# Optimization experiments

Hardware: AMD Instinct MI355X
Metric: run time of the kernel (lower is better)

The kernel has to match this reference:

```python
import jax, jax.numpy as jnp
import numpy as np

EMB = 128   # embedding_dim
ND = 128    # node_dim
B = 64      # graphs in batch
NN = 500    # n_nodes per graph
N = B * NN  # total nodes = 32000
E = 256000  # edges per edge set
M = 20      # history length in input_


def _lin_params(key, out_dim, in_dim, bias=True):
    k1, k2 = jax.random.split(key)
    s = 1.0 / np.sqrt(in_dim)
    w = jax.random.uniform(k1, (out_dim, in_dim), jnp.float32, -s, s)
    if bias:
        b = jax.random.uniform(k2, (out_dim,), jnp.float32, -s, s)
        return w, b
    return w


def setup_inputs() -> dict:
    key = jax.random.key(0)
    ks = jax.random.split(key, 40)
    inp = {}
    inp["state_"] = jax.random.normal(ks[0], (B, ND), jnp.float32)
    inp["input_"] = jax.random.normal(ks[1], (B, M, EMB), jnp.float32)
    inp["x"] = jax.random.normal(ks[2], (N, EMB), jnp.float32)
    inp["e_n"] = jax.random.randint(ks[3], (2, E), 0, N)
    inp["e_r0"] = jax.random.randint(ks[4], (2, E), 0, N)
    inp["e_r1"] = jax.random.randint(ks[5], (2, E), 0, N)
    inp["n_nodes"] = NN
    # GRU-like params
    inp["win"] = _lin_params(ks[6], ND, EMB, bias=False)
    inp["wz"], inp["bz"] = _lin_params(ks[7], ND, 2 * ND)
    inp["wr"], inp["br"] = _lin_params(ks[8], ND, 2 * ND)
    inp["wh"], inp["bh"] = _lin_params(ks[9], ND, 2 * ND)
    # GAT params: lin (out,in)+bias, attn (out, 2*out)+bias
    inp["g0_lw"], inp["g0_lb"] = _lin_params(ks[10], ND, EMB)
    inp["g0_aw"], inp["g0_ab"] = _lin_params(ks[11], ND, 2 * ND)
    inp["g1_lw"], inp["g1_lb"] = _lin_params(ks[12], ND, ND)
    inp["g1_aw"], inp["g1_ab"] = _lin_params(ks[13], ND, 2 * ND)
    inp["g2_lw"], inp["g2_lb"] = _lin_params(ks[14], ND, ND)
    inp["g2_aw"], inp["g2_ab"] = _lin_params(ks[15], ND, 2 * ND)
    inp["gn_lw"], inp["gn_lb"] = _lin_params(ks[16], ND, ND)
    inp["gn_aw"], inp["gn_ab"] = _lin_params(ks[17], ND, 2 * ND)
    # heads
    inp["pw"], inp["pb"] = _lin_params(ks[18], 1, ND)
    inp["mw"], inp["mb"] = _lin_params(ks[19], 1, ND)
    inp["sw"], inp["sb"] = _lin_params(ks[20], 1, ND)
    return inp


def gat_conv(x, ei, lw, lb, aw, ab, slope=0.2):
    """PyG GATConv variant: lin -> per-edge attn(cat(x_i,x_j)) -> leaky_relu ->
    per-dst segment softmax (per channel) -> scatter-add of x_j*alpha."""
    n = x.shape[0]
    sl = jnp.arange(n)
    src = jnp.concatenate([ei[0], sl])   # j (source)
    dst = jnp.concatenate([ei[1], sl])   # i (target; softmax + aggregation index)
    h = x @ lw.T + lb                    # [N, ND]
    hi = h[dst]                          # x_i  [E', ND]
    hj = h[src]                          # x_j  [E', ND]
    a = jnp.concatenate([hi, hj], axis=-1) @ aw.T + ab
    a = jax.nn.leaky_relu(a, slope)
    amax = jax.ops.segment_max(a, dst, num_segments=n)
    e = jnp.exp(a - amax[dst])
    denom = jax.ops.segment_sum(e, dst, num_segments=n)
    alpha = e / (denom[dst] + 1e-16)
    return jax.ops.segment_sum(hj * alpha, dst, num_segments=n)


def reference(state_, input_, x, e_n, e_r0, e_r1, n_nodes,
              win, wz, bz, wr, br, wh, bh,
              g0_lw, g0_lb, g0_aw, g0_ab,
              g1_lw, g1_lb, g1_aw, g1_ab,
              g2_lw, g2_lb, g2_aw, g2_ab,
              gn_lw, gn_lb, gn_aw, gn_ab,
              pw, pb, mw, mb, sw, sb):
    # GRU-like gated state update
    st = state_.reshape(-1, ND)
    inp = input_.reshape(st.shape[0], -1, EMB)
    i = jnp.mean(inp @ win.T, axis=1)              # [B, ND]
    si = jnp.concatenate([st, i], axis=-1)
    z = jax.nn.sigmoid(si @ wz.T + bz)
    r = jax.nn.sigmoid(si @ wr.T + br)
    hc = jnp.tanh(jnp.concatenate([r * st, i], axis=-1) @ wh.T + bh)
    h = (1 - z) * st + z * hc                      # [B, ND]

    # Stacked GAT layers
    g0 = gat_conv(x, e_n, g0_lw, g0_lb, g0_aw, g0_ab)
    g1 = gat_conv(g0, e_r1, g1_lw, g1_lb, g1_aw, g1_ab)
    g2 = gat_conv(g1, e_r1, g1_lw, g1_lb, g1_aw, g1_ab)
    g3 = gat_conv(g2, e_n, gn_lw, gn_lb, gn_aw, gn_ab) + g0
    g4 = gat_conv(g3, e_r0, g2_lw, g2_lb, g2_aw, g2_ab)
    g5 = gat_conv(g4, e_r0, g2_lw, g2_lb, g2_aw, g2_ab)
    gx = gat_conv(g5, e_n, gn_lw, gn_lb, gn_aw, gn_ab) + g3

    xg = gx.reshape(-1, n_nodes, ND)               # [B, NN, ND]
    xt = xg[:, 1:]                                 # skip depot node
    scores = (xt @ pw.T + pb)[..., 0]              # [B, NN-1]
    probs = jax.nn.softmax(scores, axis=-1)        # Categorical params
    a = jax.nn.elu((xt @ mw.T + mb)[..., 0]) + 2   # Beta alpha
    b = jax.nn.elu(jnp.abs((xt @ sw.T + sb)[..., 0])) + 2  # Beta beta
    return (h, probs, a, b)
```

## Files before the change

kernel.cpp:

```cpp
#include <hip/hip_runtime.h>
#include <hip/hip_bf16.h>

#define ND 128
#define EMB 128
#define BATCH 64
#define MM 20
#define NN 500
#define RPAD 8

typedef short bf16x8 __attribute__((ext_vector_type(8)));
typedef float f32x4 __attribute__((ext_vector_type(4)));

__device__ __forceinline__ float bf2f(unsigned short u) {
    union { unsigned int i; float f; } x; x.i = ((unsigned int)u) << 16; return x.f;
}
__device__ __forceinline__ unsigned short f2bf(float f) {
    union { float f; unsigned int i; } x; x.f = f;
    unsigned int r = x.i + 0x7fffu + ((x.i >> 16) & 1u);
    return (unsigned short)(r >> 16);
}
__device__ __forceinline__ float2 bfpair(unsigned int p) {
    union { unsigned int i; float f; } a, b;
    a.i = p << 16; b.i = p & 0xffff0000u;
    return make_float2(a.f, b.f);
}

struct EdgePtrs { const int* e[3]; };

__global__ void edge_hist3(EdgePtrs ep, int* __restrict__ cnt, int E, int N) {
    int li = blockIdx.y;
    const int* dst = ep.e[li] + E;
    int e = blockIdx.x * blockDim.x + threadIdx.x;
    if (e < E) atomicAdd(&cnt[(size_t)li * N + dst[e]], 1);
}

__global__ void exscan3(const int* __restrict__ cnt, int* __restrict__ rowptr, int n) {
    __shared__ int wsum[16];
    __shared__ int woff[16];
    int li = blockIdx.x;
    const int4* c4 = (const int4*)(cnt + (size_t)li * n);
    int* rp = rowptr + (size_t)li * (n + RPAD);
    int t = threadIdx.x;
    int lane = t & 63, wid = t >> 6;
    int n4 = n >> 2;

    int4 v[8];
    int s = 0;
#pragma unroll
    for (int i = 0; i < 8; ++i) {
        int idx = t * 8 + i;
        if (idx < n4) v[i] = c4[idx];
        else { v[i].x = v[i].y = v[i].z = v[i].w = 0; }
    }
#pragma unroll
    for (int i = 0; i < 8; ++i) s += v[i].x + v[i].y + v[i].z + v[i].w;

    int ps = s;
#pragma unroll
    for (int d = 1; d < 64; d <<= 1) {
        int u = __shfl_up(ps, d, 64);
        if (lane >= d) ps += u;
    }
    if (lane == 63) wsum[wid] = ps;
    __syncthreads();
    if (t == 0) {
        int r = 0;
        for (int i = 0; i < 16; ++i) { woff[i] = r; r += wsum[i]; }
    }
    __syncthreads();
    int run = woff[wid] + ps - s;
    int4* rp4 = (int4*)rp;
#pragma unroll
    for (int i = 0; i < 8; ++i) {
        int idx = t * 8 + i;
        if (idx < n4) {
            int4 o;
            o.x = run; run += v[i].x;
            o.y = run; run += v[i].y;
            o.z = run; run += v[i].z;
            o.w = run; run += v[i].w;
            rp4[idx] = o;
        }
    }
    if (t == (n - 1) / 32) rp[n] = run;
}

__global__ void edge_scatter3(EdgePtrs ep, const int* __restrict__ rowptr, int* __restrict__ cnt,
                              int* __restrict__ col, int E, int N) {
    int li = blockIdx.y;
    const int* src = ep.e[li];
    const int* dst = src + E;
    const int* rp = rowptr + (size_t)li * (N + RPAD);
    int e = blockIdx.x * blockDim.x + threadIdx.x;
    if (e < E) {
        int d = dst[e];
        int p = atomicSub(&cnt[(size_t)li * N + d], 1) - 1;
        col[(size_t)li * E + rp[d] + p] = src[e];
    }
}

struct WcPtrs {
    const float* lw[4]; const float* lb[4]; const float* aw[4]; const float* ab[4];
    unsigned short* Whi[4]; unsigned short* Wlo[4]; float* Bf[4];
};

__global__ void make_wc4(WcPtrs p) {
    int set = blockIdx.y;
    const float* lw = p.lw[set]; const float* lb = p.lb[set];
    const float* aw = p.aw[set]; const float* ab = p.ab[set];
    int n = blockIdx.x;
    int e = threadIdx.x;
    float w;
    if (n < 128) {
        w = lw[n * 128 + e];
    } else if (n < 256) {
        int ni = n - 128; float s = 0.f;
        for (int k = 0; k < 128; ++k) s += aw[ni * 256 + k] * lw[k * 128 + e];
        w = s;
    } else {
        int nj = n - 256; float s = 0.f;
        for (int k = 0; k < 128; ++k) s += aw[nj * 256 + 128 + k] * lw[k * 128 + e];
        w = s;
    }
    unsigned short hi = f2bf(w);
    p.Whi[set][n * 128 + e] = hi;
    p.Wlo[set][n * 128 + e] = f2bf(w - bf2f(hi));
    if (e == 0) {
        float b;
        if (n < 128) b = lb[n];
        else if (n < 256) {
            int ni = n - 128; float s = ab[ni];
            for (int k = 0; k < 128; ++k) s += aw[ni * 256 + k] * lb[k];
            b = s;
        } else {
            int nj = n - 256; float s = 0.f;
            for (int k = 0; k < 128; ++k) s += aw[nj * 256 + 128 + k] * lb[k];
            b = s;
        }
        p.Bf[set][n] = b;
    }
}

__launch_bounds__(768, 3)
__global__ void lin_fused(const float* __restrict__ X,
                          const unsigned short* __restrict__ Whi,
                          const unsigned short* __restrict__ Wlo,
                          const float* __restrict__ bias,
                          void* __restrict__ hu, int M) {
    __shared__ __align__(16) unsigned short sxh[2][16][136];
    __shared__ __align__(16) unsigned short sxl[2][16][136];
    const int tid = threadIdx.x;
    const int wave = tid >> 6;
    const int lane = tid & 63;
    const int r16 = lane & 15;
    const int quad = lane >> 4;
    const int srow = tid >> 4;
    const int scol = (tid & 15) * 8;

    unsigned short* hu16 = (unsigned short*)hu;
    float* huf = (float*)hu;

    bf16x8 wh[2][4], wl[2][4];
#pragma unroll
    for (int nt = 0; nt < 2; ++nt)
#pragma unroll
        for (int ks = 0; ks < 4; ++ks) {
            size_t wrow = (size_t)(wave * 32 + nt * 16 + r16) * 128 + ks * 32 + quad * 8;
            wh[nt][ks] = *(const bf16x8*)(Whi + wrow);
            wl[nt][ks] = *(const bf16x8*)(Wlo + wrow);
        }
    float bv[2];
#pragma unroll
    for (int nt = 0; nt < 2; ++nt) bv[nt] = bias[wave * 32 + nt * 16 + r16];

    const int mt_count = M >> 4;
    const int G = gridDim.x;
    const int mt0 = blockIdx.x;

    {
        float v[8];
        if (tid < 256) {
            const float* xp = X + (size_t)(mt0 * 16 + srow) * 128 + scol;
            float4 v0 = *(const float4*)xp;
            float4 v1 = *(const float4*)(xp + 4);
            v[0] = v0.x; v[1] = v0.y; v[2] = v0.z; v[3] = v0.w;
            v[4] = v1.x; v[5] = v1.y; v[6] = v1.z; v[7] = v1.w;
            unsigned int hh[4], ll[4];
#pragma unroll
            for (int j = 0; j < 4; ++j) {
                unsigned short h0 = f2bf(v[2 * j]);
                unsigned short h1 = f2bf(v[2 * j + 1]);
                unsigned short l0 = f2bf(v[2 * j] - bf2f(h0));
                unsigned short l1 = f2bf(v[2 * j + 1] - bf2f(h1));
                hh[j] = (unsigned int)h0 | ((unsigned int)h1 << 16);
                ll[j] = (unsigned int)l0 | ((unsigned int)l1 << 16);
            }
            *(uint4*)&sxh[0][srow][scol] = make_uint4(hh[0], hh[1], hh[2], hh[3]);
            *(uint4*)&sxl[0][srow][scol] = make_uint4(ll[0], ll[1], ll[2], ll[3]);
        }
    }
    __syncthreads();

    int cur = 0;
    for (int mt = mt0; mt < mt_count; mt += G) {
        const int nxt = mt + G;
        const bool has = nxt < mt_count;

        float v[8];
        if (has && tid < 256) {
            const float* xp = X + (size_t)(nxt * 16 + srow) * 128 + scol;
            float4 v0 = *(const float4*)xp;
            float4 v1 = *(const float4*)(xp + 4);
            v[0] = v0.x; v[1] = v0.y; v[2] = v0.z; v[3] = v0.w;
            v[4] = v1.x; v[5] = v1.y; v[6] = v1.z; v[7] = v1.w;
        }

        bf16x8 ah[4], al[4];
#pragma unroll
        for (int ks = 0; ks < 4; ++ks) {
            ah[ks] = *(const bf16x8*)&sxh[cur][r16][ks * 32 + quad * 8];
            al[ks] = *(const bf16x8*)&sxl[cur][r16][ks * 32 + quad * 8];
        }

#pragma unroll
        for (int nt = 0; nt < 2; ++nt) {
            f32x4 acc = {bv[nt], bv[nt], bv[nt], bv[nt]};
#pragma unroll
            for (int ks = 0; ks < 4; ++ks) {
                acc = __builtin_amdgcn_mfma_f32_16x16x32_bf16(ah[ks], wh[nt][ks], acc, 0, 0, 0);
                acc = __builtin_amdgcn_mfma_f32_16x16x32_bf16(al[ks], wh[nt][ks], acc, 0, 0, 0);
                acc = __builtin_amdgcn_mfma_f32_16x16x32_bf16(ah[ks], wl[nt][ks], acc, 0, 0, 0);
            }
            int cc = wave * 32 + nt * 16 + r16;
#pragma unroll
            for (int r = 0; r < 4; ++r) {
                size_t row = (size_t)(mt * 16 + quad * 4 + r);
                if (cc < 128) {
                    hu16[row * 512 + ((cc & ~1) << 1) + (cc & 1)] = f2bf(acc[r]);
                } else if (cc < 256) {
                    int c = cc - 128;
                    huf[row * 256 + 128 + c] = acc[r];
                } else {
                    int c = cc - 256;
                    hu16[row * 512 + ((c & ~1) << 1) + 2 + (c & 1)] = f2bf(acc[r]);
                }
            }
        }

        if (has && tid < 256) {
            unsigned int hh[4], ll[4];
#pragma unroll
            for (int j = 0; j < 4; ++j) {
                unsigned short h0 = f2bf(v[2 * j]);
                unsigned short h1 = f2bf(v[2 * j + 1]);
                unsigned short l0 = f2bf(v[2 * j] - bf2f(h0));
                unsigned short l1 = f2bf(v[2 * j + 1] - bf2f(h1));
                hh[j] = (unsigned int)h0 | ((unsigned int)h1 << 16);
                ll[j] = (unsigned int)l0 | ((unsigned int)l1 << 16);
            }
            *(uint4*)&sxh[cur ^ 1][srow][scol] = make_uint4(hh[0], hh[1], hh[2], hh[3]);
            *(uint4*)&sxl[cur ^ 1][srow][scol] = make_uint4(ll[0], ll[1], ll[2], ll[3]);
        }
        __syncthreads();
        cur ^= 1;
    }
}

__global__ void gat_agg(const void* __restrict__ hu,
                        const int* __restrict__ rowptr, const int* __restrict__ col,
                        const float* __restrict__ resid,
                        float* __restrict__ out, int N) {
    int wid = (int)((blockIdx.x * blockDim.x + threadIdx.x) >> 6);
    if (wid >= N) return;
    int lane = threadIdx.x & 63;
    const uint2* P = (const uint2*)hu;
    const float2* U = (const float2*)hu;

    float2 uiv = U[(size_t)wid * 128 + 64 + lane];
    uint2 sp = P[(size_t)wid * 128 + lane];
    float2 hs = bfpair(sp.x);
    float2 ujs = bfpair(sp.y);

    float a0 = uiv.x + ujs.x; a0 = a0 > 0.f ? a0 : 0.2f * a0;
    float a1 = uiv.y + ujs.y; a1 = a1 > 0.f ? a1 : 0.2f * a1;
    float m0 = a0, m1 = a1, l0 = 1.f, l1 = 1.f;
    float acc0 = hs.x, acc1 = hs.y;

#define AGG_STEP(pk)                                                      \
    {                                                                     \
        float2 hj = bfpair(pk.x);                                         \
        float2 uj = bfpair(pk.y);                                         \
        float b0 = uiv.x + uj.x; b0 = b0 > 0.f ? b0 : 0.2f * b0;          \
        float b1 = uiv.y + uj.y; b1 = b1 > 0.f ? b1 : 0.2f * b1;          \
        float n0 = fmaxf(m0, b0), n1 = fmaxf(m1, b1);                     \
        float s0 = __expf(m0 - n0), s1 = __expf(m1 - n1);                 \
        float p0 = __expf(b0 - n0), p1 = __expf(b1 - n1);                 \
        l0 = l0 * s0 + p0;            l1 = l1 * s1 + p1;                  \
        acc0 = acc0 * s0 + hj.x * p0; acc1 = acc1 * s1 + hj.y * p1;       \
        m0 = n0; m1 = n1;                                                 \
    }

    int e = rowptr[wid], end = rowptr[wid + 1];
    for (; e + 8 <= end; e += 8) {
        int s0i = col[e],     s1i = col[e + 1], s2i = col[e + 2], s3i = col[e + 3];
        int s4i = col[e + 4], s5i = col[e + 5], s6i = col[e + 6], s7i = col[e + 7];
        uint2 p0 = P[(size_t)s0i * 128 + lane];
        uint2 p1 = P[(size_t)s1i * 128 + lane];
        uint2 p2 = P[(size_t)s2i * 128 + lane];
        uint2 p3 = P[(size_t)s3i * 128 + lane];
        uint2 p4 = P[(size_t)s4i * 128 + lane];
        uint2 p5 = P[(size_t)s5i * 128 + lane];
        uint2 p6 = P[(size_t)s6i * 128 + lane];
        uint2 p7 = P[(size_t)s7i * 128 + lane];
        AGG_STEP(p0);
        AGG_STEP(p1);
        AGG_STEP(p2);
        AGG_STEP(p3);
        AGG_STEP(p4);
        AGG_STEP(p5);
        AGG_STEP(p6);
        AGG_STEP(p7);
    }
    for (; e + 4 <= end; e += 4) {
        int sA = col[e], sB = col[e + 1], sC = col[e + 2], sD = col[e + 3];
        uint2 pA = P[(size_t)sA * 128 + lane];
        uint2 pB = P[(size_t)sB * 128 + lane];
        uint2 pC = P[(size_t)sC * 128 + lane];
        uint2 pD = P[(size_t)sD * 128 + lane];
        AGG_STEP(pA);
        AGG_STEP(pB);
        AGG_STEP(pC);
        AGG_STEP(pD);
    }
    for (; e < end; ++e) {
        int sA = col[e];
        uint2 pA = P[(size_t)sA * 128 + lane];
        AGG_STEP(pA);
    }
#undef AGG_STEP

    float o0 = acc0 / (l0 + 1e-16f);
    float o1 = acc1 / (l1 + 1e-16f);
    if (resid) {
        float2 rv = ((const float2*)resid)[(size_t)wid * 64 + lane];
        o0 += rv.x; o1 += rv.y;
    }
    ((float2*)out)[(size_t)wid * 64 + lane] = make_float2(o0, o1);
}

__global__ void gru_kernel(const float* __restrict__ st_, const float* __restrict__ in_,
                           const float* __restrict__ win,
                           const float* __restrict__ wz, const float* __restrict__ bz,
                           const float* __restrict__ wr, const float* __restrict__ br,
                           const float* __restrict__ wh, const float* __restrict__ bh,
                           float* __restrict__ out) {
    __shared__ float sst[ND], sib[EMB], si[ND], srs[ND];
    int b = blockIdx.x, d = threadIdx.x;
    float s = 0.f;
    for (int m = 0; m < MM; ++m) s += in_[((size_t)b * MM + m) * EMB + d];
    sib[d] = s * (1.0f / MM);
    sst[d] = st_[b * ND + d];
    __syncthreads();
    float iv = 0.f;
    for (int e = 0; e < EMB; ++e) iv += sib[e] * win[d * EMB + e];
    si[d] = iv;
    __syncthreads();
    float za = bz[d], ra = br[d];
    for (int e = 0; e < ND; ++e) {
        za += sst[e] * wz[d * 2 * ND + e] + si[e] * wz[d * 2 * ND + ND + e];
        ra += sst[e] * wr[d * 2 * ND + e] + si[e] * wr[d * 2 * ND + ND + e];
    }
    float z = 1.f / (1.f + __expf(-za));
    float r = 1.f / (1.f + __expf(-ra));
    srs[d] = r * sst[d];
    __syncthreads();
    float ha = bh[d];
    for (int e = 0; e < ND; ++e)
        ha += srs[e] * wh[d * 2 * ND + e] + si[e] * wh[d * 2 * ND + ND + e];
    float hc = tanhf(ha);
    out[b * ND + d] = (1.f - z) * sst[d] + z * hc;
}

__global__ void heads_dots(const float* __restrict__ gx,
                           const float* __restrict__ pw_,
                           const float* __restrict__ mw_, const float* __restrict__ mb_,
                           const float* __restrict__ sw_, const float* __restrict__ sbias_,
                           float* __restrict__ scores, float* __restrict__ out) {
    int t = blockIdx.x;
    int lane = threadIdx.x & 63;
    int b = blockIdx.y * 4 + (threadIdx.x >> 6);
    const float2* g2 = (const float2*)gx;
    float2 pwv = ((const float2*)pw_)[lane];
    float2 mwv = ((const float2*)mw_)[lane];
    float2 swv = ((const float2*)sw_)[lane];
    int node = b * NN + 1 + t;
    float2 xv = g2[(size_t)node * 64 + lane];
    float dp = xv.x * pwv.x + xv.y * pwv.y;
    float dm = xv.x * mwv.x + xv.y * mwv.y;
    float ds = xv.x * swv.x + xv.y * swv.y;
    for (int off = 32; off; off >>= 1) {
        dp += __shfl_xor(dp, off);
        dm += __shfl_xor(dm, off);
        ds += __shfl_xor(ds, off);
    }
    if (lane == 0) {
        scores[(size_t)b * (NN - 1) + t] = dp;
        float av = dm + mb_[0]; av = av > 0.f ? av : (__expf(av) - 1.f);
        float bv = fabsf(ds + sbias_[0]);
        float* oA = out + BATCH * ND + (size_t)BATCH * (NN - 1);
        float* oB = oA + (size_t)BATCH * (NN - 1);
        oA[(size_t)b * (NN - 1) + t] = av + 2.f;
        oB[(size_t)b * (NN - 1) + t] = bv + 2.f;
    }
}

__global__ void heads_softmax(const float* __restrict__ scores, float* __restrict__ out) {
    __shared__ float scs[NN - 1], red[256];
    int b = blockIdx.x, tid = threadIdx.x;
    float mx = -1e30f;
    for (int t = tid; t < NN - 1; t += 256) { float v = scores[(size_t)b * (NN - 1) + t]; scs[t] = v; mx = fmaxf(mx, v); }
    red[tid] = mx; __syncthreads();
    for (int off = 128; off; off >>= 1) { if (tid < off) red[tid] = fmaxf(red[tid], red[tid + off]); __syncthreads(); }
    mx = red[0]; __syncthreads();
    float sum = 0.f;
    for (int t = tid; t < NN - 1; t += 256) { float e = __expf(scs[t] - mx); scs[t] = e; sum += e; }
    red[tid] = sum; __syncthreads();
    for (int off = 128; off; off >>= 1) { if (tid < off) red[tid] += red[tid + off]; __syncthreads(); }
    float inv = 1.0f / red[0];
    float* oP = out + BATCH * ND + (size_t)b * (NN - 1);
    for (int t = tid; t < NN - 1; t += 256) oP[t] = scs[t] * inv;
}

extern "C" void kernel_launch(void* const* d_in, const int* in_sizes, int n_in,
                              void* d_out, int out_size, void* d_ws, size_t ws_size,
                              hipStream_t stream) {
    const float* state_ = (const float*)d_in[0];
    const float* input_ = (const float*)d_in[1];
    const float* x      = (const float*)d_in[2];
    const int* e_n  = (const int*)d_in[3];
    const int* e_r0 = (const int*)d_in[4];
    const int* e_r1 = (const int*)d_in[5];
    const float* win = (const float*)d_in[7];
    const float* wz  = (const float*)d_in[8];
    const float* bz  = (const float*)d_in[9];
    const float* wr  = (const float*)d_in[10];
    const float* br  = (const float*)d_in[11];
    const float* wh  = (const float*)d_in[12];
    const float* bh  = (const float*)d_in[13];
    const float* pw = (const float*)d_in[30];
    const float* mw = (const float*)d_in[32];
    const float* mb = (const float*)d_in[33];
    const float* sw = (const float*)d_in[34];
    const float* sb = (const float*)d_in[35];
    float* out = (float*)d_out;

    const int E = in_sizes[3] / 2;
    const int N = in_sizes[2] / EMB;

    char* w = (char*)d_ws;
    auto alloc = [&](size_t bytes) { char* p = w; w += (bytes + 255) & ~(size_t)255; return p; };
    int* rpbase = (int*)alloc(3 * (size_t)(N + RPAD) * sizeof(int));
    int* colbase = (int*)alloc(3 * (size_t)E * sizeof(int));
    int* tmp = (int*)alloc(3 * (size_t)N * sizeof(int));
    unsigned short* Whi[4]; unsigned short* Wlo[4]; float* Bf[4];
    for (int i = 0; i < 4; ++i) {
        Whi[i] = (unsigned short*)alloc(384 * 128 * 2);
        Wlo[i] = (unsigned short*)alloc(384 * 128 * 2);
        Bf[i]  = (float*)alloc(384 * 4);
    }
    void* hu = (void*)alloc((size_t)N * 1024);
    float* ga = (float*)alloc((size_t)N * 128 * 4);
    float* gb = (float*)alloc((size_t)N * 128 * 4);
    float* gc = (float*)alloc((size_t)N * 128 * 4);
    float* scores = (float*)alloc((size_t)BATCH * (NN - 1) * 4);

    EdgePtrs ep; ep.e[0] = e_n; ep.e[1] = e_r0; ep.e[2] = e_r1;

    hipMemsetAsync(tmp, 0, 3 * (size_t)N * sizeof(int), stream);
    edge_hist3<<<dim3((E + 255) / 256, 3), 256, 0, stream>>>(ep, tmp, E, N);
    exscan3<<<3, 1024, 0, stream>>>(tmp, rpbase, N);
    edge_scatter3<<<dim3((E + 255) / 256, 3), 256, 0, stream>>>(ep, rpbase, tmp, colbase, E, N);

    WcPtrs wp;
    wp.lw[0] = (const float*)d_in[14]; wp.lb[0] = (const float*)d_in[15];
    wp.aw[0] = (const float*)d_in[16]; wp.ab[0] = (const float*)d_in[17];
    wp.lw[1] = (const float*)d_in[18]; wp.lb[1] = (const float*)d_in[19];
    wp.aw[1] = (const float*)d_in[20]; wp.ab[1] = (const float*)d_in[21];
    wp.lw[2] = (const float*)d_in[22]; wp.lb[2] = (const float*)d_in[23];
    wp.aw[2] = (const float*)d_in[24]; wp.ab[2] = (const float*)d_in[25];
    wp.lw[3] = (const float*)d_in[26]; wp.lb[3] = (const float*)d_in[27];
    wp.aw[3] = (const float*)d_in[28]; wp.ab[3] = (const float*)d_in[29];
    for (int i = 0; i < 4; ++i) { wp.Whi[i] = Whi[i]; wp.Wlo[i] = Wlo[i]; wp.Bf[i] = Bf[i]; }
    make_wc4<<<dim3(384, 4), 128, 0, stream>>>(wp);

    gru_kernel<<<BATCH, ND, 0, stream>>>(state_, input_, win, wz, bz, wr, br, wh, bh, out);

    auto conv = [&](const float* in, int csr_i, int wi, const float* resid, float* o) {
        lin_fused<<<512, 768, 0, stream>>>(in, Whi[wi], Wlo[wi], Bf[wi], hu, N);
        gat_agg<<<(N * 64) / 256, 256, 0, stream>>>(hu, rpbase + (size_t)csr_i * (N + RPAD),
                                                    colbase + (size_t)csr_i * E, resid, o, N);
    };

    conv(x,  0, 0, nullptr, ga);
    conv(ga, 2, 1, nullptr, gb);
    conv(gb, 2, 1, nullptr, gc);
    conv(gc, 0, 3, ga,      gb);
    conv(gb, 1, 2, nullptr, gc);
    conv(gc, 1, 2, nullptr, ga);
    conv(ga, 0, 3, gb,      gc);

    heads_dots<<<dim3(NN - 1, 16), 256, 0, stream>>>(gc, pw, mw, mb, sw, sb, scores, out);
    heads_softmax<<<BATCH, 256, 0, stream>>>(scores, out);
}
```

Measured before the change: 613.0 us.

## Split each GAT aggregation wave into two half-waves over interleaved edges with 16-byte loads

The aggregation kernel now splits each 64-lane wave into two 32-lane halves. Each half walks alternate edges of the destination node and loads 16 bytes per lane instead of 8. The two halves keep separate online-softmax state and merge it with a cross-half shuffle before writing. The intent is more independent gathers in flight with wider loads. The cost is extra per-lane state, a merge step, and idle lanes during the final store.

```diff
diff --git a/kernel.cpp b/kernel.cpp
--- a/kernel.cpp
+++ b/kernel.cpp
@@ -273,79 +273,92 @@
     int wid = (int)((blockIdx.x * blockDim.x + threadIdx.x) >> 6);
     if (wid >= N) return;
     int lane = threadIdx.x & 63;
-    const uint2* P = (const uint2*)hu;
-    const float2* U = (const float2*)hu;
-
-    float2 uiv = U[(size_t)wid * 128 + 64 + lane];
-    uint2 sp = P[(size_t)wid * 128 + lane];
-    float2 hs = bfpair(sp.x);
-    float2 ujs = bfpair(sp.y);
-
-    float a0 = uiv.x + ujs.x; a0 = a0 > 0.f ? a0 : 0.2f * a0;
-    float a1 = uiv.y + ujs.y; a1 = a1 > 0.f ? a1 : 0.2f * a1;
-    float m0 = a0, m1 = a1, l0 = 1.f, l1 = 1.f;
-    float acc0 = hs.x, acc1 = hs.y;
-
-#define AGG_STEP(pk)                                                      \
-    {                                                                     \
-        float2 hj = bfpair(pk.x);                                         \
-        float2 uj = bfpair(pk.y);                                         \
-        float b0 = uiv.x + uj.x; b0 = b0 > 0.f ? b0 : 0.2f * b0;          \
-        float b1 = uiv.y + uj.y; b1 = b1 > 0.f ? b1 : 0.2f * b1;          \
-        float n0 = fmaxf(m0, b0), n1 = fmaxf(m1, b1);                     \
-        float s0 = __expf(m0 - n0), s1 = __expf(m1 - n1);                 \
-        float p0 = __expf(b0 - n0), p1 = __expf(b1 - n1);                 \
-        l0 = l0 * s0 + p0;            l1 = l1 * s1 + p1;                  \
-        acc0 = acc0 * s0 + hj.x * p0; acc1 = acc1 * s1 + hj.y * p1;       \
-        m0 = n0; m1 = n1;                                                 \
-    }
-
-    int e = rowptr[wid], end = rowptr[wid + 1];
-    for (; e + 8 <= end; e += 8) {
-        int s0i = col[e],     s1i = col[e + 1], s2i = col[e + 2], s3i = col[e + 3];
-        int s4i = col[e + 4], s5i = col[e + 5], s6i = col[e + 6], s7i = col[e + 7];
-        uint2 p0 = P[(size_t)s0i * 128 + lane];
-        uint2 p1 = P[(size_t)s1i * 128 + lane];
-        uint2 p2 = P[(size_t)s2i * 128 + lane];
-        uint2 p3 = P[(size_t)s3i * 128 + lane];
-        uint2 p4 = P[(size_t)s4i * 128 + lane];
-        uint2 p5 = P[(size_t)s5i * 128 + lane];
-        uint2 p6 = P[(size_t)s6i * 128 + lane];
-        uint2 p7 = P[(size_t)s7i * 128 + lane];
-        AGG_STEP(p0);
-        AGG_STEP(p1);
-        AGG_STEP(p2);
-        AGG_STEP(p3);
-        AGG_STEP(p4);
-        AGG_STEP(p5);
-        AGG_STEP(p6);
-        AGG_STEP(p7);
-    }
-    for (; e + 4 <= end; e += 4) {
-        int sA = col[e], sB = col[e + 1], sC = col[e + 2], sD = col[e + 3];
-        uint2 pA = P[(size_t)sA * 128 + lane];
-        uint2 pB = P[(size_t)sB * 128 + lane];
-        uint2 pC = P[(size_t)sC * 128 + lane];
-        uint2 pD = P[(size_t)sD * 128 + lane];
-        AGG_STEP(pA);
-        AGG_STEP(pB);
-        AGG_STEP(pC);
-        AGG_STEP(pD);
-    }
-    for (; e < end; ++e) {
-        int sA = col[e];
-        uint2 pA = P[(size_t)sA * 128 + lane];
-        AGG_STEP(pA);
-    }
-#undef AGG_STEP
-
-    float o0 = acc0 / (l0 + 1e-16f);
-    float o1 = acc1 / (l1 + 1e-16f);
-    if (resid) {
-        float2 rv = ((const float2*)resid)[(size_t)wid * 64 + lane];
-        o0 += rv.x; o1 += rv.y;
-    }
-    ((float2*)out)[(size_t)wid * 64 + lane] = make_float2(o0, o1);
+    int half = lane >> 5;
+    int j = lane & 31;
+    const uint4* P = (const uint4*)hu;
+
+    float4 uiv = *(const float4*)((const char*)hu + (size_t)wid * 1024 + 512 + j * 16);
+
+    float m[4], l[4], acc[4];
+    if (half == 0) {
+        uint4 sp = P[(size_t)wid * 64 + j];
+        float2 h01 = bfpair(sp.x), u01 = bfpair(sp.y);
+        float2 h23 = bfpair(sp.z), u23 = bfpair(sp.w);
+        float a0 = uiv.x + u01.x; a0 = a0 > 0.f ? a0 : 0.2f * a0;
+        float a1 = uiv.y + u01.y; a1 = a1 > 0.f ? a1 : 0.2f * a1;
+        float a2 = uiv.z + u23.x; a2 = a2 > 0.f ? a2 : 0.2f * a2;
+        float a3 = uiv.w + u23.y; a3 = a3 > 0.f ? a3 : 0.2f * a3;
+        m[0] = a0; m[1] = a1; m[2] = a2; m[3] = a3;
+        l[0] = l[1] = l[2] = l[3] = 1.f;
+        acc[0] = h01.x; acc[1] = h01.y; acc[2] = h23.x; acc[3] = h23.y;
+    } else {
+#pragma unroll
+        for (int c = 0; c < 4; ++c) { m[c] = -1e30f; l[c] = 0.f; acc[c] = 0.f; }
+    }
+
+#define AGG_STEP4(pk)                                                         \
+    {                                                                         \
+        float2 h01 = bfpair(pk.x), u01 = bfpair(pk.y);                        \
+        float2 h23 = bfpair(pk.z), u23 = bfpair(pk.w);                        \
+        float b[4] = {uiv.x + u01.x, uiv.y + u01.y, uiv.z + u23.x, uiv.w + u23.y}; \
+        float hj[4] = {h01.x, h01.y, h23.x, h23.y};                           \
+        _Pragma("unroll")                                                     \
+        for (int c = 0; c < 4; ++c) {                                         \
+            float bb = b[c] > 0.f ? b[c] : 0.2f * b[c];                       \
+            float nm = fmaxf(m[c], bb);                                       \
+            float s = __expf(m[c] - nm);                                      \
+            float p = __expf(bb - nm);                                        \
+            l[c] = l[c] * s + p;                                              \
+            acc[c] = acc[c] * s + hj[c] * p;                                  \
+            m[c] = nm;                                                        \
+        }                                                                     \
+    }
+
+    int e0 = rowptr[wid], end = rowptr[wid + 1];
+    int eh = e0 + half;
+    for (; eh + 6 < end; eh += 8) {
+        int sA = col[eh], sB = col[eh + 2], sC = col[eh + 4], sD = col[eh + 6];
+        uint4 pA = P[(size_t)sA * 64 + j];
+        uint4 pB = P[(size_t)sB * 64 + j];
+        uint4 pC = P[(size_t)sC * 64 + j];
+        uint4 pD = P[(size_t)sD * 64 + j];
+        AGG_STEP4(pA);
+        AGG_STEP4(pB);
+        AGG_STEP4(pC);
+        AGG_STEP4(pD);
+    }
+    for (; eh < end; eh += 2) {
+        int sA = col[eh];
+        uint4 pA = P[(size_t)sA * 64 + j];
+        AGG_STEP4(pA);
+    }
+#undef AGG_STEP4
+
+#pragma unroll
+    for (int c = 0; c < 4; ++c) {
+        float mo = __shfl_xor(m[c], 32);
+        float lo = __shfl_xor(l[c], 32);
+        float ao = __shfl_xor(acc[c], 32);
+        float nm = fmaxf(m[c], mo);
+        float s0 = __expf(m[c] - nm);
+        float s1 = __expf(mo - nm);
+        l[c] = l[c] * s0 + lo * s1;
+        acc[c] = acc[c] * s0 + ao * s1;
+        m[c] = nm;
+    }
+
+    if (half == 0) {
+        float4 o;
+        o.x = acc[0] / (l[0] + 1e-16f);
+        o.y = acc[1] / (l[1] + 1e-16f);
+        o.z = acc[2] / (l[2] + 1e-16f);
+        o.w = acc[3] / (l[3] + 1e-16f);
+        if (resid) {
+            float4 rv = *(const float4*)(resid + (size_t)wid * 128 + j * 4);
+            o.x += rv.x; o.y += rv.y; o.z += rv.z; o.w += rv.w;
+        }
+        *(float4*)(out + (size_t)wid * 128 + j * 4) = o;
+    }
 }
 
 __global__ void gru_kernel(const float* __restrict__ st_, const float* __restrict__ in_,
```

After: 668.4 us. 9.0% more time.
